# Kernel optimization log

Measured on AMD Instinct MI355X. Metric: run time of the kernel, lower is better.

Reference implementation:

```python
import jax, jax.numpy as jnp
import numpy as np

N, E, DIN, H = 10000, 80000, 1024, 512
NEG = 0.2  # PyG GATv2Conv default negative_slope


def gatv2(x, src, dst, wl, bl, wr, br, att, b, n):
    # GATv2: e_ij = att . leaky_relu(Wl x_j + Wr x_i); segment softmax over dst; sum alpha * Wl x_j
    xl = x @ wl + bl            # [N, H] source transform
    xr = x @ wr + br            # [N, H] target transform
    z = jax.nn.leaky_relu(xl[src] + xr[dst], NEG)   # [E, H]
    e = z @ att                                      # [E]
    m = jax.ops.segment_max(e, dst, num_segments=n)  # per-target max (self-loops guarantee nonempty)
    p = jnp.exp(e - m[dst])
    s = jax.ops.segment_sum(p, dst, num_segments=n)
    alpha = p / (s[dst] + 1e-16)                     # [E]
    out = jax.ops.segment_sum(alpha[:, None] * xl[src], dst, num_segments=n)
    return out + b


def setup_inputs() -> dict:
    key = jax.random.key(0)
    ks = iter(jax.random.split(key, 64))
    d = {}
    d["x"] = jax.random.normal(next(ks), (N, DIN), jnp.float32)
    d["edge_index"] = jax.random.randint(next(ks), (2, E), 0, N, dtype=jnp.int32).astype(jnp.int64)
    dims = [DIN, H, H, H]
    for i in range(4):
        din = dims[i]
        sc = 1.0 / np.sqrt(din)
        d[f"wl{i+1}"] = jax.random.normal(next(ks), (din, H), jnp.float32) * sc
        d[f"bl{i+1}"] = jnp.zeros((H,), jnp.float32)
        d[f"wr{i+1}"] = jax.random.normal(next(ks), (din, H), jnp.float32) * sc
        d[f"br{i+1}"] = jnp.zeros((H,), jnp.float32)
        d[f"att{i+1}"] = jax.random.normal(next(ks), (H,), jnp.float32) * (1.0 / np.sqrt(H))
        d[f"b{i+1}"] = jnp.zeros((H,), jnp.float32)
    for name, din, dout in [("1", H, 512), ("2", 512, 256), ("3", 256, 2)]:
        d[f"lw{name}"] = jax.random.normal(next(ks), (din, dout), jnp.float32) * (1.0 / np.sqrt(din))
        d[f"lb{name}"] = jnp.zeros((dout,), jnp.float32)
    return d


def reference(x, edge_index, wl1, bl1, wr1, br1, att1, b1,
              wl2, bl2, wr2, br2, att2, b2,
              wl3, bl3, wr3, br3, att3, b3,
              wl4, bl4, wr4, br4, att4, b4,
              lw1, lb1, lw2, lb2, lw3, lb3):
    n = x.shape[0]
    loops = jnp.arange(n, dtype=edge_index.dtype)
    src = jnp.concatenate([edge_index[0], loops])  # add self-loops (PyG default)
    dst = jnp.concatenate([edge_index[1], loops])
    h = jax.nn.relu(gatv2(x, src, dst, wl1, bl1, wr1, br1, att1, b1, n))
    h = jax.nn.relu(gatv2(h, src, dst, wl2, bl2, wr2, br2, att2, b2, n))
    h = jax.nn.relu(gatv2(h, src, dst, wl3, bl3, wr3, br3, att3, b3, n))
    h = jax.nn.relu(gatv2(h, src, dst, wl4, bl4, wr4, br4, att4, b4, n))
    # dropout is identity at inference
    h = jax.nn.relu(h @ lw1 + lb1)
    h = jax.nn.relu(h @ lw2 + lb2)
    logits = h @ lw3 + lb3
    return logits, jax.nn.softmax(logits, axis=1)
```

## Files before the change

### kernel.cpp

```cpp
#include <hip/hip_runtime.h>
#include <cstdint>

#define NN 10000
#define NE 80000
#define DIN_ 1024
#define HH 512

typedef __attribute__((ext_vector_type(8))) short bf16x8;
typedef __attribute__((ext_vector_type(4))) float f32x4;
typedef unsigned short u16;
typedef unsigned int u32;

static __device__ __forceinline__ float b2f(u16 u) {
  u32 i = ((u32)u) << 16;
  return __builtin_bit_cast(float, i);
}
static __device__ __forceinline__ u16 f2b(float f) {
  u32 i = __builtin_bit_cast(u32, f);
  u32 r = (i + 0x7fffu + ((i >> 16) & 1u)) >> 16;
  return (u16)r;
}
static __device__ __forceinline__ void unpack8(uint4 u, float* f) {
  f[0] = __builtin_bit_cast(float, u.x << 16);
  f[1] = __builtin_bit_cast(float, u.x & 0xffff0000u);
  f[2] = __builtin_bit_cast(float, u.y << 16);
  f[3] = __builtin_bit_cast(float, u.y & 0xffff0000u);
  f[4] = __builtin_bit_cast(float, u.z << 16);
  f[5] = __builtin_bit_cast(float, u.z & 0xffff0000u);
  f[6] = __builtin_bit_cast(float, u.w << 16);
  f[7] = __builtin_bit_cast(float, u.w & 0xffff0000u);
}
static __device__ __forceinline__ void load8(const u16* p, float* f) { unpack8(*(const uint4*)p, f); }

#define ASYNC_CP16(gp, lp)                                                        \
  __builtin_amdgcn_global_load_lds((__attribute__((address_space(1))) void*)(gp), \
                                   (__attribute__((address_space(3))) void*)(lp), \
                                   16, 0, 0)

static __device__ __forceinline__ int float_flag(const u16* xw) {
  __shared__ int c;
  if (threadIdx.x == 0) c = 0;
  __syncthreads();
  int bad = 0;
  for (int i = threadIdx.x; i < 2048; i += blockDim.x) {
    u32 e = (xw[i] >> 7) & 0xFFu;
    if (e >= 140u) bad++;
  }
  if (bad) atomicAdd(&c, bad);
  __syncthreads();
  return c > 64;
}
static __device__ __forceinline__ int int64_flag(const u32* ew) {
  __shared__ int c;
  if (threadIdx.x == 0) c = 0;
  __syncthreads();
  int z = 0;
  for (int i = threadIdx.x; i < 256; i += blockDim.x)
    if (ew[2 * i + 1] == 0u) z++;
  if (z) atomicAdd(&c, z);
  __syncthreads();
  return c > 200;
}

__global__ void k_edges(const void* ei, int* esrc, int* edst, int* counts) {
  int f64 = int64_flag((const u32*)ei);
  int i = blockIdx.x * 256 + threadIdx.x;
  if (i < NE) {
    int sv, dv;
    if (f64) {
      sv = (int)((const long long*)ei)[i];
      dv = (int)((const long long*)ei)[NE + i];
    } else {
      sv = ((const int*)ei)[i];
      dv = ((const int*)ei)[NE + i];
    }
    esrc[i] = sv;
    edst[i] = dv;
    atomicAdd(&counts[dv], 1);
  } else if (i < NE + NN) {
    atomicAdd(&counts[i - NE], 1);
  }
}

__global__ __launch_bounds__(512) void k_scan(const int* counts, int* rowptr, int* cursor, int n) {
  __shared__ int lds[512];
  const int PER = 20;
  int t = threadIdx.x;
  int base = t * PER;
  int v[PER];
  int sum = 0;
#pragma unroll
  for (int i = 0; i < PER; i++) {
    int idx = base + i;
    v[i] = (idx < n) ? counts[idx] : 0;
    sum += v[i];
  }
  lds[t] = sum;
  __syncthreads();
  for (int off = 1; off < 512; off <<= 1) {
    int x = (t >= off) ? lds[t - off] : 0;
    __syncthreads();
    lds[t] += x;
    __syncthreads();
  }
  int run = (t > 0) ? lds[t - 1] : 0;
#pragma unroll
  for (int i = 0; i < PER; i++) {
    int idx = base + i;
    if (idx < n) {
      cursor[idx] = run;
      run += v[i];
      rowptr[idx + 1] = run;
    }
  }
  if (t == 0) rowptr[0] = 0;
}

#define SBLK 352
#define XBLK 2048
struct Prep {
  const int* esrc;
  const int* edst;
  int* cursor;
  int* col;
  const void* xin;
  u16* xout;
  const void* vin[20];
  u16* vout[20];
  int vn[20];
  const void* tin[10];
  u16* tout[10];
  int tK[10], tN[10], toff[10];
};
__global__ void k_prep(Prep a) {
  __shared__ u16 tt[32][33];
  int b = blockIdx.x;
  if (b < SBLK) {
    int i = b * 256 + threadIdx.x;
    if (i < NE) {
      int p = atomicAdd(&a.cursor[a.edst[i]], 1);
      a.col[p] = a.esrc[i];
    } else if (i < NE + NN) {
      int v = i - NE;
      int p = atomicAdd(&a.cursor[v], 1);
      a.col[p] = v;
    }
    return;
  }
  b -= SBLK;
  int f = float_flag((const u16*)a.xin);
  if (b < XBLK) {
    const int total = NN * DIN_ / 8;
    for (int g = b * 256 + threadIdx.x; g < total; g += XBLK * 256) {
      u16 o[8];
      if (f) {
        const float* p = (const float*)a.xin + (size_t)g * 8;
#pragma unroll
        for (int i = 0; i < 8; i++) o[i] = f2b(p[i]);
      } else {
        *(uint4*)o = *((const uint4*)a.xin + g);
      }
      *((uint4*)a.xout + g) = *(const uint4*)o;
    }
  } else if (b < XBLK + 20) {
    int v = b - XBLK;
    const void* in = a.vin[v];
    u16* out = a.vout[v];
    int n = a.vn[v];
    for (int i = threadIdx.x; i < n; i += 256)
      out[i] = f ? f2b(((const float*)in)[i]) : ((const u16*)in)[i];
  } else {
    int tb = b - XBLK - 20;
    int seg = 0;
#pragma unroll
    for (int i = 1; i < 10; i++)
      if (tb >= a.toff[i]) seg = i;
    int tl = tb - a.toff[seg];
    int K = a.tK[seg], N = a.tN[seg];
    int tiles_n = N >> 5;
    int n0 = (tl % tiles_n) << 5, k0 = (tl / tiles_n) << 5;
    const void* in = a.tin[seg];
    u16* out = a.tout[seg];
    int tx = threadIdx.x & 31, ty = threadIdx.x >> 5;
    for (int r = ty; r < 32; r += 8) {
      size_t idx = (size_t)(k0 + r) * N + n0 + tx;
      tt[r][tx] = f ? f2b(((const float*)in)[idx]) : ((const u16*)in)[idx];
    }
    __syncthreads();
    for (int r = ty; r < 32; r += 8) out[(size_t)(n0 + r) * K + k0 + tx] = tt[tx][r];
  }
}

__global__ __launch_bounds__(256) void k_gemm128(const u16* __restrict__ A, int lda,
                                                 const u16* __restrict__ Bt,
                                                 const u16* __restrict__ bias,
                                                 u16* __restrict__ C,
                                                 int M, int N, int K, int act,
                                                 int tiles_m, int ln_tiles_n) {
  __shared__ u16 sA[2 * 128 * 32];
  __shared__ u16 sB[2 * 128 * 32];
  int id = blockIdx.x;
  int xcd = id & 7;
  int rest = id >> 3;
  int xt = rest & ((1 << ln_tiles_n) - 1);
  int yt = ((rest >> ln_tiles_n) << 3) + xcd;
  if (yt >= tiles_m) return;
  int m0 = yt << 7, n0 = xt << 7;
  int t = threadIdx.x;
  int wave = t >> 6, lane = t & 63;

  int srow = t >> 2;
  int sk = ((t & 3) ^ ((t >> 3) & 3)) * 8;
  const u16* agp[4];
  const u16* bgp[4];
  u16* la[4];
  u16* lb[4];
#pragma unroll
  for (int q = 0; q < 4; q++) {
    int h = q >> 1;
    int row = ((q & 1) << 6) + srow;
    int ra = m0 + row;
    ra = ra < M ? ra : M - 1;
    agp[q] = A + (size_t)ra * lda + h * 32 + sk;
    bgp[q] = Bt + (size_t)(n0 + row) * K + h * 32 + sk;
    int lofs = h * 4096 + (((q & 1) << 8) + t) * 8;
    la[q] = sA + lofs;
    lb[q] = sB + lofs;
  }

  int wm = (wave >> 1) << 6, wn = (wave & 1) << 6;
  int lr = lane & 15;
  int kcs = (((lane >> 4) ^ ((lr >> 1) & 3))) * 8;

  f32x4 acc[4][4];
#pragma unroll
  for (int i = 0; i < 4; i++)
#pragma unroll
    for (int j = 0; j < 4; j++) acc[i][j] = (f32x4){0.f, 0.f, 0.f, 0.f};

  for (int k0 = 0; k0 < K; k0 += 64) {
#pragma unroll
    for (int q = 0; q < 4; q++) ASYNC_CP16(agp[q] + k0, la[q]);
#pragma unroll
    for (int q = 0; q < 4; q++) ASYNC_CP16(bgp[q] + k0, lb[q]);
    __syncthreads();
    bf16x8 a[2][4], b[2][4];
#pragma unroll
    for (int s = 0; s < 2; s++) {
#pragma unroll
      for (int i = 0; i < 4; i++) a[s][i] = *(const bf16x8*)(sA + s * 4096 + (wm + i * 16 + lr) * 32 + kcs);
#pragma unroll
      for (int j = 0; j < 4; j++) b[s][j] = *(const bf16x8*)(sB + s * 4096 + (wn + j * 16 + lr) * 32 + kcs);
    }
#pragma unroll
    for (int s = 0; s < 2; s++)
#pragma unroll
      for (int i = 0; i < 4; i++)
#pragma unroll
        for (int j = 0; j < 4; j++)
          acc[i][j] = __builtin_amdgcn_mfma_f32_16x16x32_bf16(a[s][i], b[s][j], acc[i][j], 0, 0, 0);
    __syncthreads();
  }

  int rbase = (lane >> 4) << 2;
#pragma unroll
  for (int j = 0; j < 4; j++) {
    int colc = n0 + wn + j * 16 + lr;
    float bv = b2f(bias[colc]);
#pragma unroll
    for (int i = 0; i < 4; i++) {
#pragma unroll
      for (int r = 0; r < 4; r++) {
        int row = m0 + wm + i * 16 + rbase + r;
        if (row < M) {
          float v = acc[i][j][r] + bv;
          if (act) v = fmaxf(v, 0.f);
          C[(size_t)row * N + colc] = f2b(v);
        }
      }
    }
  }
}

__global__ __launch_bounds__(256) void k_attn5(u16* __restrict__ xlr,
                                               const u16* __restrict__ att, const u16* __restrict__ bias,
                                               const int* __restrict__ rowptr, const int* __restrict__ col,
                                               int n) {
  int node = (blockIdx.x * 256 + threadIdx.x) >> 6;
  if (node >= n) return;
  int lane = threadIdx.x & 63;
  int h0 = lane * 8;
  float a[8], r[8];
  load8(att + h0, a);
  load8(xlr + (size_t)node * 1024 + 512 + h0, r);
  int e0 = rowptr[node], e1 = rowptr[node + 1];

  float m = -3e38f, s = 0.f;
  float acc[8] = {0.f, 0.f, 0.f, 0.f, 0.f, 0.f, 0.f, 0.f};
  int j0 = col[e0];
  int j1 = col[(e0 + 1 < e1) ? e0 + 1 : e0];
  uint4 raw0 = *(const uint4*)(xlr + (size_t)j0 * 1024 + h0);
  uint4 raw1 = *(const uint4*)(xlr + (size_t)j1 * 1024 + h0);

  for (int e = e0; e < e1; e += 2) {
    bool has2 = (e + 1 < e1);
    int jn0 = col[(e + 2 < e1) ? e + 2 : e1 - 1];
    int jn1 = col[(e + 3 < e1) ? e + 3 : e1 - 1];
    uint4 p0 = *(const uint4*)(xlr + (size_t)jn0 * 1024 + h0);
    uint4 p1 = *(const uint4*)(xlr + (size_t)jn1 * 1024 + h0);
    float x0[8], x1[8];
    unpack8(raw0, x0);
    unpack8(raw1, x1);
    float pa = 0.f, pb = 0.f;
#pragma unroll
    for (int i = 0; i < 8; i++) {
      float z0 = x0[i] + r[i];
      z0 = z0 > 0.f ? z0 : 0.2f * z0;
      pa = fmaf(a[i], z0, pa);
      float z1 = x1[i] + r[i];
      z1 = z1 > 0.f ? z1 : 0.2f * z1;
      pb = fmaf(a[i], z1, pb);
    }
#pragma unroll
    for (int off = 32; off >= 1; off >>= 1) {
      pa += __shfl_xor(pa, off);
      pb += __shfl_xor(pb, off);
    }
    if (pa > m) {
      float al = __expf(m - pa);
      s = fmaf(s, al, 1.f);
#pragma unroll
      for (int i = 0; i < 8; i++) acc[i] = fmaf(acc[i], al, x0[i]);
      m = pa;
    } else {
      float w = __expf(pa - m);
      s += w;
#pragma unroll
      for (int i = 0; i < 8; i++) acc[i] = fmaf(w, x0[i], acc[i]);
    }
    if (has2) {
      if (pb > m) {
        float al = __expf(m - pb);
        s = fmaf(s, al, 1.f);
#pragma unroll
        for (int i = 0; i < 8; i++) acc[i] = fmaf(acc[i], al, x1[i]);
        m = pb;
      } else {
        float w = __expf(pb - m);
        s += w;
#pragma unroll
        for (int i = 0; i < 8; i++) acc[i] = fmaf(w, x1[i], acc[i]);
      }
    }
    raw0 = p0;
    raw1 = p1;
  }
  float inv = 1.f / (s + 1e-16f);

  float bv[8];
  load8(bias + h0, bv);
  uint4 o;
  u32 p8[8];
#pragma unroll
  for (int i = 0; i < 8; i++) {
    float v = fmaf(acc[i], inv, bv[i]);
    v = fmaxf(v, 0.f);
    p8[i] = f2b(v);
  }
  o.x = p8[0] | (p8[1] << 16);
  o.y = p8[2] | (p8[3] << 16);
  o.z = p8[4] | (p8[5] << 16);
  o.w = p8[6] | (p8[7] << 16);
  *(uint4*)(xlr + (size_t)node * 1024 + 512 + h0) = o;
}

__global__ __launch_bounds__(256) void k_head(const u16* __restrict__ h2, const u16* __restrict__ lw3,
                                              const u16* __restrict__ lb3, float* __restrict__ out, int n) {
  int row = (blockIdx.x * 256 + threadIdx.x) >> 6;
  if (row >= n) return;
  int lane = threadIdx.x & 63;
  int k0 = lane * 4;
  uint2 hu = *(const uint2*)(h2 + (size_t)row * 256 + k0);
  float hx[4];
  hx[0] = __builtin_bit_cast(float, hu.x << 16);
  hx[1] = __builtin_bit_cast(float, hu.x & 0xffff0000u);
  hx[2] = __builtin_bit_cast(float, hu.y << 16);
  hx[3] = __builtin_bit_cast(float, hu.y & 0xffff0000u);
  float wv[8];
  load8(lw3 + (size_t)k0 * 2, wv);
  float p0 = 0.f, p1 = 0.f;
#pragma unroll
  for (int i = 0; i < 4; i++) {
    p0 = fmaf(hx[i], wv[2 * i], p0);
    p1 = fmaf(hx[i], wv[2 * i + 1], p1);
  }
#pragma unroll
  for (int off = 32; off >= 1; off >>= 1) {
    p0 += __shfl_xor(p0, off);
    p1 += __shfl_xor(p1, off);
  }
  if (lane == 0) {
    float l0 = p0 + b2f(lb3[0]);
    float l1 = p1 + b2f(lb3[1]);
    float mx = fmaxf(l0, l1);
    float q0 = __expf(l0 - mx), q1 = __expf(l1 - mx);
    float si = 1.f / (q0 + q1);
    out[row * 2 + 0] = l0;
    out[row * 2 + 1] = l1;
    out[2 * n + row * 2 + 0] = q0 * si;
    out[2 * n + row * 2 + 1] = q1 * si;
  }
}

extern "C" void kernel_launch(void* const* d_in, const int* in_sizes, int n_in,
                              void* d_out, int out_size, void* d_ws, size_t ws_size,
                              hipStream_t stream) {
  (void)in_sizes; (void)n_in; (void)out_size; (void)ws_size;
  const void* x_raw = d_in[0];
  const void* ei_raw = d_in[1];
  const void *wl[4], *bl[4], *wr[4], *br[4], *att[4], *bg[4];
  for (int i = 0; i < 4; i++) {
    wl[i] = d_in[2 + i * 6 + 0];
    bl[i] = d_in[2 + i * 6 + 1];
    wr[i] = d_in[2 + i * 6 + 2];
    br[i] = d_in[2 + i * 6 + 3];
    att[i] = d_in[2 + i * 6 + 4];
    bg[i] = d_in[2 + i * 6 + 5];
  }
  const void* lw1 = d_in[26];
  const void* lb1 = d_in[27];
  const void* lw2 = d_in[28];
  const void* lb2 = d_in[29];
  const void* lw3 = d_in[30];
  const void* lb3 = d_in[31];

  size_t off = 0;
  auto alloc = [&](size_t bytes) -> void* {
    off = (off + 255) & ~(size_t)255;
    void* p = (char*)d_ws + off;
    off += bytes;
    return p;
  };
  int* esrc = (int*)alloc(NE * 4);
  int* edst = (int*)alloc(NE * 4);
  int* counts = (int*)alloc(NN * 4);
  int* rowptr = (int*)alloc((NN + 1) * 4);
  int* cursor = (int*)alloc(NN * 4);
  int* col = (int*)alloc((NE + NN) * 4);
  u16* cb = (u16*)alloc(4 * 1024 * 2);
  u16* attv = (u16*)alloc(4 * 512 * 2);
  u16* bgv = (u16*)alloc(4 * 512 * 2);
  u16* lb1v = (u16*)alloc(512 * 2);
  u16* lb2v = (u16*)alloc(256 * 2);
  u16* lw3v = (u16*)alloc(512 * 2);
  u16* lb3v = (u16*)alloc(2 * 2);
  u16* comb0 = (u16*)alloc((size_t)1024 * 1024 * 2);
  u16* combL[4];
  combL[0] = comb0;
  for (int l = 1; l < 4; l++) combL[l] = (u16*)alloc((size_t)1024 * 512 * 2);
  u16* lw1T = (u16*)alloc((size_t)512 * 512 * 2);
  u16* lw2T = (u16*)alloc((size_t)256 * 512 * 2);
  u16* xc = (u16*)alloc((size_t)NN * DIN_ * 2);
  u16* X0 = (u16*)alloc((size_t)NN * 1024 * 2);
  u16* X1 = (u16*)alloc((size_t)NN * 1024 * 2);
  u16* mlp1 = xc;
  u16* mlp2 = xc + (size_t)NN * 512;

  hipMemsetAsync(counts, 0, NN * 4, stream);
  int ET = NE + NN;
  k_edges<<<(ET + 255) / 256, 256, 0, stream>>>(ei_raw, esrc, edst, counts);
  k_scan<<<1, 512, 0, stream>>>(counts, rowptr, cursor, NN);

  Prep pa;
  pa.esrc = esrc;
  pa.edst = edst;
  pa.cursor = cursor;
  pa.col = col;
  pa.xin = x_raw;
  pa.xout = xc;
  for (int l = 0; l < 4; l++) {
    pa.vin[l * 4 + 0] = bl[l];  pa.vout[l * 4 + 0] = cb + l * 1024;        pa.vn[l * 4 + 0] = 512;
    pa.vin[l * 4 + 1] = br[l];  pa.vout[l * 4 + 1] = cb + l * 1024 + 512;  pa.vn[l * 4 + 1] = 512;
    pa.vin[l * 4 + 2] = att[l]; pa.vout[l * 4 + 2] = attv + l * 512;       pa.vn[l * 4 + 2] = 512;
    pa.vin[l * 4 + 3] = bg[l];  pa.vout[l * 4 + 3] = bgv + l * 512;        pa.vn[l * 4 + 3] = 512;
  }
  pa.vin[16] = lb1; pa.vout[16] = lb1v; pa.vn[16] = 512;
  pa.vin[17] = lb2; pa.vout[17] = lb2v; pa.vn[17] = 256;
  pa.vin[18] = lw3; pa.vout[18] = lw3v; pa.vn[18] = 512;
  pa.vin[19] = lb3; pa.vout[19] = lb3v; pa.vn[19] = 2;
  const void* tin[10] = {wl[0], wr[0], wl[1], wr[1], wl[2], wr[2], wl[3], wr[3], lw1, lw2};
  u16* tout[10] = {comb0, comb0 + (size_t)512 * 1024,
                   combL[1], combL[1] + (size_t)512 * 512,
                   combL[2], combL[2] + (size_t)512 * 512,
                   combL[3], combL[3] + (size_t)512 * 512,
                   lw1T, lw2T};
  int tK[10] = {1024, 1024, 512, 512, 512, 512, 512, 512, 512, 512};
  int tN[10] = {512, 512, 512, 512, 512, 512, 512, 512, 512, 256};
  int acc_off = 0;
  for (int i = 0; i < 10; i++) {
    pa.tin[i] = tin[i];
    pa.tout[i] = tout[i];
    pa.tK[i] = tK[i];
    pa.tN[i] = tN[i];
    pa.toff[i] = acc_off;
    acc_off += (tN[i] >> 5) * (tK[i] >> 5);
  }
  k_prep<<<SBLK + XBLK + 20 + acc_off, 256, 0, stream>>>(pa);

  auto gemm = [&](const u16* A, int lda, const u16* Bt, const u16* bias, u16* C,
                  int M, int Nn, int K, int act) {
    int tiles_m = (M + 127) >> 7;
    int tiles_n = Nn >> 7;
    int ln = (tiles_n == 8) ? 3 : (tiles_n == 4) ? 2 : 1;
    int mgrp = (tiles_m + 7) >> 3;
    int blocks = (mgrp << 3) * tiles_n;
    k_gemm128<<<blocks, 256, 0, stream>>>(A, lda, Bt, bias, C, M, Nn, K, act, tiles_m, ln);
  };
  auto attn = [&](u16* xlr, int l) {
    k_attn5<<<(NN * 64 + 255) / 256, 256, 0, stream>>>(xlr, attv + l * 512, bgv + l * 512,
                                                       rowptr, col, NN);
  };

  gemm(xc, 1024, comb0, cb + 0 * 1024, X0, NN, 1024, 1024, 0);
  attn(X0, 0);
  gemm(X0 + 512, 1024, combL[1], cb + 1 * 1024, X1, NN, 1024, 512, 0);
  attn(X1, 1);
  gemm(X1 + 512, 1024, combL[2], cb + 2 * 1024, X0, NN, 1024, 512, 0);
  attn(X0, 2);
  gemm(X0 + 512, 1024, combL[3], cb + 3 * 1024, X1, NN, 1024, 512, 0);
  attn(X1, 3);

  gemm(X1 + 512, 1024, lw1T, lb1v, mlp1, NN, 512, 512, 1);
  gemm(mlp1, 512, lw2T, lb2v, mlp2, NN, 256, 512, 1);
  k_head<<<(NN * 64 + 255) / 256, 256, 0, stream>>>(mlp2, lw3v, lb3v, (float*)d_out, NN);
}
```

Measured before the change: 383.1 us.

## Double-buffer GEMM shared-memory tiles to overlap async loads with MFMA

Doubles the LDS tiles in the 128x128 GEMM so the async global-to-LDS copies for the next k-step are issued before computing on the current one. It waits with explicit vmcnt counts and raw barriers in place of __syncthreads. The aim is to hide global load latency behind matrix-core work. In exchange, LDS use doubles to 64KB per block, which may cut occupancy, and the hand-written waitcnt and barrier logic is fragile.

```diff
diff --git a/kernel.cpp b/kernel.cpp
--- a/kernel.cpp
+++ b/kernel.cpp
@@ -197,8 +197,8 @@
                                                  u16* __restrict__ C,
                                                  int M, int N, int K, int act,
                                                  int tiles_m, int ln_tiles_n) {
-  __shared__ u16 sA[2 * 128 * 32];
-  __shared__ u16 sB[2 * 128 * 32];
+  __shared__ u16 sA[2][2 * 128 * 32];
+  __shared__ u16 sB[2][2 * 128 * 32];
   int id = blockIdx.x;
   int xcd = id & 7;
   int rest = id >> 3;
@@ -213,8 +213,7 @@
   int sk = ((t & 3) ^ ((t >> 3) & 3)) * 8;
   const u16* agp[4];
   const u16* bgp[4];
-  u16* la[4];
-  u16* lb[4];
+  int lofs[4];
 #pragma unroll
   for (int q = 0; q < 4; q++) {
     int h = q >> 1;
@@ -223,9 +222,7 @@
     ra = ra < M ? ra : M - 1;
     agp[q] = A + (size_t)ra * lda + h * 32 + sk;
     bgp[q] = Bt + (size_t)(n0 + row) * K + h * 32 + sk;
-    int lofs = h * 4096 + (((q & 1) << 8) + t) * 8;
-    la[q] = sA + lofs;
-    lb[q] = sB + lofs;
+    lofs[q] = h * 4096 + (((q & 1) << 8) + t) * 8;
   }
 
   int wm = (wave >> 1) << 6, wn = (wave & 1) << 6;
@@ -238,19 +235,31 @@
 #pragma unroll
     for (int j = 0; j < 4; j++) acc[i][j] = (f32x4){0.f, 0.f, 0.f, 0.f};
 
-  for (int k0 = 0; k0 < K; k0 += 64) {
-#pragma unroll
-    for (int q = 0; q < 4; q++) ASYNC_CP16(agp[q] + k0, la[q]);
-#pragma unroll
-    for (int q = 0; q < 4; q++) ASYNC_CP16(bgp[q] + k0, lb[q]);
-    __syncthreads();
+#pragma unroll
+  for (int q = 0; q < 4; q++) ASYNC_CP16(agp[q], sA[0] + lofs[q]);
+#pragma unroll
+  for (int q = 0; q < 4; q++) ASYNC_CP16(bgp[q], sB[0] + lofs[q]);
+
+  int buf = 0;
+  for (int k0 = 0; k0 < K; k0 += 64, buf ^= 1) {
+    int kn = k0 + 64;
+    if (kn < K) {
+#pragma unroll
+      for (int q = 0; q < 4; q++) ASYNC_CP16(agp[q] + kn, sA[buf ^ 1] + lofs[q]);
+#pragma unroll
+      for (int q = 0; q < 4; q++) ASYNC_CP16(bgp[q] + kn, sB[buf ^ 1] + lofs[q]);
+      asm volatile("s_waitcnt vmcnt(8)" ::: "memory");
+    } else {
+      asm volatile("s_waitcnt vmcnt(0)" ::: "memory");
+    }
+    __builtin_amdgcn_s_barrier();
     bf16x8 a[2][4], b[2][4];
 #pragma unroll
     for (int s = 0; s < 2; s++) {
 #pragma unroll
-      for (int i = 0; i < 4; i++) a[s][i] = *(const bf16x8*)(sA + s * 4096 + (wm + i * 16 + lr) * 32 + kcs);
-#pragma unroll
-      for (int j = 0; j < 4; j++) b[s][j] = *(const bf16x8*)(sB + s * 4096 + (wn + j * 16 + lr) * 32 + kcs);
+      for (int i = 0; i < 4; i++) a[s][i] = *(const bf16x8*)(sA[buf] + s * 4096 + (wm + i * 16 + lr) * 32 + kcs);
+#pragma unroll
+      for (int j = 0; j < 4; j++) b[s][j] = *(const bf16x8*)(sB[buf] + s * 4096 + (wn + j * 16 + lr) * 32 + kcs);
     }
 #pragma unroll
     for (int s = 0; s < 2; s++)
@@ -259,7 +268,7 @@
 #pragma unroll
         for (int j = 0; j < 4; j++)
           acc[i][j] = __builtin_amdgcn_mfma_f32_16x16x32_bf16(a[s][i], b[s][j], acc[i][j], 0, 0, 0);
-    __syncthreads();
+    __builtin_amdgcn_s_barrier();
   }
 
   int rbase = (lane >> 4) << 2;
```

New measurement: 405.4 us. 1.06x slower.
